# Performance work log

Hardware: AMD Instinct MI355X
Metric: run time of the kernel (lower is better)

The kernel has to match this reference:

```python
import jax, jax.numpy as jnp
import numpy as np

NUM_NODES = 200000
NUM_EDGES = 200000
NUM_GRAPHS = 2048
F_IN = 128
H = 64


def setup_inputs() -> dict:
    key = jax.random.key(0)
    ks = jax.random.split(key, 16)
    x = jax.random.normal(ks[0], (NUM_NODES, F_IN), dtype=jnp.float32)
    edge_index = jax.random.randint(ks[1], (2, NUM_EDGES), 0, NUM_NODES, dtype=jnp.int64)
    batch = jnp.sort(jax.random.randint(ks[2], (NUM_NODES,), 0, NUM_GRAPHS, dtype=jnp.int64))
    s_in = 1.0 / np.sqrt(F_IN)
    s_h = 1.0 / np.sqrt(H)
    W1a = jax.random.uniform(ks[3], (F_IN, H), jnp.float32, -s_in, s_in)
    b1a = jax.random.uniform(ks[4], (H,), jnp.float32, -s_in, s_in)
    W1b = jax.random.uniform(ks[5], (H, H), jnp.float32, -s_h, s_h)
    b1b = jax.random.uniform(ks[6], (H,), jnp.float32, -s_h, s_h)
    W2a = jax.random.uniform(ks[7], (H, H), jnp.float32, -s_h, s_h)
    b2a = jax.random.uniform(ks[8], (H,), jnp.float32, -s_h, s_h)
    W2b = jax.random.uniform(ks[9], (H, H), jnp.float32, -s_h, s_h)
    b2b = jax.random.uniform(ks[10], (H,), jnp.float32, -s_h, s_h)
    fcW = jax.random.uniform(ks[11], (H, 1), jnp.float32, -s_h, s_h)
    fcb = jax.random.uniform(ks[12], (1,), jnp.float32, -s_h, s_h)
    return {"x": x, "edge_index": edge_index, "batch": batch,
            "W1a": W1a, "b1a": b1a, "W1b": W1b, "b1b": b1b,
            "W2a": W2a, "b2a": b2a, "W2b": W2b, "b2b": b2b,
            "fcW": fcW, "fcb": fcb}


def gin_conv(h, edge_index, Wa, ba, Wb, bb):
    # sum aggregation: messages from source (row 0) scattered to target (row 1)
    msgs = h[edge_index[0]]  # [E, D]
    agg = jax.ops.segment_sum(msgs, edge_index[1], num_segments=NUM_NODES)
    z = h + agg  # eps = 0 default: (1+eps)*x + sum_j x_j
    z = jnp.maximum(z @ Wa + ba, 0.0)
    return z @ Wb + bb


def reference(x, edge_index, batch, W1a, b1a, W1b, b1b, W2a, b2a, W2b, b2b, fcW, fcb):
    h = jnp.maximum(gin_conv(x, edge_index, W1a, b1a, W1b, b1b), 0.0)
    h = jnp.maximum(gin_conv(h, edge_index, W2a, b2a, W2b, b2b), 0.0)
    # global mean pool per graph
    sums = jax.ops.segment_sum(h, batch, num_segments=NUM_GRAPHS)  # [G, H]
    counts = jax.ops.segment_sum(jnp.ones((h.shape[0],), h.dtype), batch, num_segments=NUM_GRAPHS)
    pooled = sums / jnp.maximum(counts, 1.0)[:, None]
    out = pooled @ fcW + fcb  # [G, 1]
    return out.squeeze(-1)
```

## Files before the change

kernel.cpp:

```cpp
#include <hip/hip_runtime.h>
#include <hip/hip_bf16.h>


#define NODES 200000
#define NPAD  200064
#define EDGES 200000
#define GRAPHS 2048
#define NB_SCAN 782

typedef __attribute__((ext_vector_type(8))) short short8;
typedef __attribute__((ext_vector_type(4))) short short4v;
typedef __attribute__((ext_vector_type(4))) float f32x4;

__device__ __forceinline__ unsigned short f2bf(float f) {
    unsigned u = __builtin_bit_cast(unsigned, f);
    u = (u + 0x7fffu + ((u >> 16) & 1u)) >> 16;
    return (unsigned short)u;
}
__device__ __forceinline__ float bf2f(unsigned short h) {
    unsigned u = ((unsigned)h) << 16;
    return __builtin_bit_cast(float, u);
}

__global__ __launch_bounds__(256) void count_k(
    const int* __restrict__ ei, int* __restrict__ cnt, int E)
{
    int e = blockIdx.x * 256 + threadIdx.x;
    if (e < E) atomicAdd(&cnt[ei[E + e]], 1);
}

__global__ __launch_bounds__(256) void scan1_k(
    const int* __restrict__ cnt, int* __restrict__ excl,
    int* __restrict__ bsum, int N)
{
    __shared__ int sh[256];
    int tid = threadIdx.x;
    int i = blockIdx.x * 256 + tid;
    int v = (i < N) ? cnt[i] : 0;
    sh[tid] = v;
    __syncthreads();
    for (int off = 1; off < 256; off <<= 1) {
        int t = (tid >= off) ? sh[tid - off] : 0;
        __syncthreads();
        sh[tid] += t;
        __syncthreads();
    }
    if (i < N) excl[i] = sh[tid] - v;
    if (tid == 255) bsum[blockIdx.x] = sh[255];
}

__global__ __launch_bounds__(1024) void scan2_k(int* __restrict__ bsum, int NB)
{
    __shared__ int sh[1024];
    int tid = threadIdx.x;
    int v = (tid < NB) ? bsum[tid] : 0;
    sh[tid] = v;
    __syncthreads();
    for (int off = 1; off < 1024; off <<= 1) {
        int t = (tid >= off) ? sh[tid - off] : 0;
        __syncthreads();
        sh[tid] += t;
        __syncthreads();
    }
    if (tid < NB) bsum[tid] = sh[tid] - v;
}

__global__ __launch_bounds__(256) void scan3_k(
    int* __restrict__ rowptr, const int* __restrict__ bsum,
    int* __restrict__ cursor, int N, int E)
{
    int i = blockIdx.x * 256 + threadIdx.x;
    if (i < N) {
        int v = rowptr[i] + bsum[blockIdx.x];
        rowptr[i] = v;
        cursor[i] = v;
    }
    if (i == 0) rowptr[N] = E;
}

__global__ __launch_bounds__(256) void fill_k(
    const int* __restrict__ ei, int* __restrict__ cursor,
    int* __restrict__ srcs, int E)
{
    int e = blockIdx.x * 256 + threadIdx.x;
    if (e < E) {
        int d = ei[E + e];
        int p = atomicAdd(&cursor[d], 1);
        srcs[p] = ei[e];
    }
}

__device__ __forceinline__ void wconv(const float* __restrict__ W,
                                      short* __restrict__ F, int e, int NE)
{
    int lane = e & 63, nb = (e >> 6) & 3, kc = e >> 8;
    int col = nb * 16 + (lane & 15);
    int kb = kc * 32 + ((lane >> 4) * 8);
    short8 hi, lo;
    #pragma unroll
    for (int j = 0; j < 8; ++j) {
        float w = W[(size_t)(kb + j) * 64 + col];
        unsigned short h = f2bf(w);
        float r = w - bf2f(h);
        hi[j] = (short)h;
        lo[j] = (short)f2bf(r);
    }
    *reinterpret_cast<short8*>(F + (size_t)e * 8) = hi;
    *reinterpret_cast<short8*>(F + (size_t)NE * 8 + (size_t)e * 8) = lo;
}

__global__ __launch_bounds__(256) void wsplit_k(
    const float* __restrict__ W1a, const float* __restrict__ W1b,
    const float* __restrict__ W2a, const float* __restrict__ W2b,
    short* __restrict__ F1a, short* __restrict__ F1b,
    short* __restrict__ F2a, short* __restrict__ F2b)
{
    int t = blockIdx.x * 256 + threadIdx.x;
    if (t < 1024)      wconv(W1a, F1a, t, 1024);
    else if (t < 1536) wconv(W1b, F1b, t - 1024, 512);
    else if (t < 2048) wconv(W2a, F2a, t - 1536, 512);
    else if (t < 2560) wconv(W2b, F2b, t - 2048, 512);
}

__device__ __forceinline__ void cvt_a8(const float4& a, const float4& b,
                                       short8& hi, short8& lo)
{
    float av[8] = {a.x, a.y, a.z, a.w, b.x, b.y, b.z, b.w};
    #pragma unroll
    for (int j = 0; j < 8; ++j) {
        unsigned short h = f2bf(av[j]);
        float r = av[j] - bf2f(h);
        hi[j] = (short)h;
        lo[j] = (short)f2bf(r);
    }
}

__global__ __launch_bounds__(256) void mm1_k(
    const float* __restrict__ A, const short* __restrict__ Wf,
    float* __restrict__ out, int N)
{
    const int tid = threadIdx.x;
    const int lane = tid & 63;
    const int wv = tid >> 6;
    const int row0w = blockIdx.x * 128 + wv * 32;
    const int grp = lane >> 4, c = lane & 15;
    const int koff = grp * 8;

    const float* Ar0 = A + (size_t)min(row0w + c, N - 1) * 128;
    const float* Ar1 = A + (size_t)min(row0w + 16 + c, N - 1) * 128;

    f32x4 acc[2][4];
    #pragma unroll
    for (int rg = 0; rg < 2; ++rg)
        #pragma unroll
        for (int nb = 0; nb < 4; ++nb)
            acc[rg][nb] = (f32x4){0.f, 0.f, 0.f, 0.f};

    #pragma unroll
    for (int kc = 0; kc < 4; ++kc) {
        const int kb = kc * 32 + koff;
        float4 a00 = *reinterpret_cast<const float4*>(Ar0 + kb);
        float4 a01 = *reinterpret_cast<const float4*>(Ar0 + kb + 4);
        float4 a10 = *reinterpret_cast<const float4*>(Ar1 + kb);
        float4 a11 = *reinterpret_cast<const float4*>(Ar1 + kb + 4);
        short8 h0, l0, h1, l1;
        cvt_a8(a00, a01, h0, l0);
        cvt_a8(a10, a11, h1, l1);
        #pragma unroll
        for (int nb = 0; nb < 4; ++nb) {
            short8 whi = *reinterpret_cast<const short8*>(Wf + ((size_t)((kc * 4 + nb) * 64) + lane) * 8);
            short8 wlo = *reinterpret_cast<const short8*>(Wf + ((size_t)(1024 + (kc * 4 + nb) * 64) + lane) * 8);
            acc[0][nb] = __builtin_amdgcn_mfma_f32_16x16x32_bf16(h0, whi, acc[0][nb], 0, 0, 0);
            acc[0][nb] = __builtin_amdgcn_mfma_f32_16x16x32_bf16(l0, whi, acc[0][nb], 0, 0, 0);
            acc[0][nb] = __builtin_amdgcn_mfma_f32_16x16x32_bf16(h0, wlo, acc[0][nb], 0, 0, 0);
            acc[1][nb] = __builtin_amdgcn_mfma_f32_16x16x32_bf16(h1, whi, acc[1][nb], 0, 0, 0);
            acc[1][nb] = __builtin_amdgcn_mfma_f32_16x16x32_bf16(l1, whi, acc[1][nb], 0, 0, 0);
            acc[1][nb] = __builtin_amdgcn_mfma_f32_16x16x32_bf16(h1, wlo, acc[1][nb], 0, 0, 0);
        }
    }

    #pragma unroll
    for (int rg = 0; rg < 2; ++rg)
        #pragma unroll
        for (int nb = 0; nb < 4; ++nb)
            #pragma unroll
            for (int reg = 0; reg < 4; ++reg)
                out[(size_t)(row0w + rg * 16 + grp * 4 + reg) * 64 + nb * 16 + c] = acc[rg][nb][reg];
}

__global__ __launch_bounds__(256) void agg_split_k(
    const float* __restrict__ y, const int* __restrict__ rowptr,
    const int* __restrict__ srcs, const float* __restrict__ bias,
    short* __restrict__ zHi, short* __restrict__ zLo, int N)
{
    int t = blockIdx.x * 256 + threadIdx.x;
    int node = t >> 4;
    if (node >= N) return;
    int c = (t & 15) * 4;

    int s0 = rowptr[node];
    int s1 = rowptr[node + 1];

    float4 acc = *reinterpret_cast<const float4*>(y + (size_t)node * 64 + c);
    float4 b4 = *reinterpret_cast<const float4*>(bias + c);
    acc.x += b4.x; acc.y += b4.y; acc.z += b4.z; acc.w += b4.w;

    for (int j = s0; j < s1; ++j) {
        int s = srcs[j];
        float4 vv = *reinterpret_cast<const float4*>(y + (size_t)s * 64 + c);
        acc.x += vv.x; acc.y += vv.y; acc.z += vv.z; acc.w += vv.w;
    }

    float v[4] = {fmaxf(acc.x, 0.f), fmaxf(acc.y, 0.f),
                  fmaxf(acc.z, 0.f), fmaxf(acc.w, 0.f)};
    short4v hv, lv;
    #pragma unroll
    for (int i = 0; i < 4; ++i) {
        unsigned short h = f2bf(v[i]);
        float r = v[i] - bf2f(h);
        hv[i] = (short)h;
        lv[i] = (short)f2bf(r);
    }
    *reinterpret_cast<short4v*>(zHi + (size_t)node * 64 + c) = hv;
    *reinterpret_cast<short4v*>(zLo + (size_t)node * 64 + c) = lv;
}

__device__ __forceinline__ void mm64_core(
    const short* __restrict__ zHi, const short* __restrict__ zLo,
    const short* __restrict__ Wf, int row0w, int lane, f32x4 acc[2][4])
{
    const int grp = lane >> 4, c = lane & 15;
    const int koff = grp * 8;
    const short* zh0 = zHi + (size_t)(row0w + c) * 64;
    const short* zl0 = zLo + (size_t)(row0w + c) * 64;
    const short* zh1 = zHi + (size_t)(row0w + 16 + c) * 64;
    const short* zl1 = zLo + (size_t)(row0w + 16 + c) * 64;

    #pragma unroll
    for (int kc = 0; kc < 2; ++kc) {
        const int kb = kc * 32 + koff;
        short8 h0 = *reinterpret_cast<const short8*>(zh0 + kb);
        short8 l0 = *reinterpret_cast<const short8*>(zl0 + kb);
        short8 h1 = *reinterpret_cast<const short8*>(zh1 + kb);
        short8 l1 = *reinterpret_cast<const short8*>(zl1 + kb);
        #pragma unroll
        for (int nb = 0; nb < 4; ++nb) {
            short8 whi = *reinterpret_cast<const short8*>(Wf + ((size_t)((kc * 4 + nb) * 64) + lane) * 8);
            short8 wlo = *reinterpret_cast<const short8*>(Wf + ((size_t)(512 + (kc * 4 + nb) * 64) + lane) * 8);
            acc[0][nb] = __builtin_amdgcn_mfma_f32_16x16x32_bf16(h0, whi, acc[0][nb], 0, 0, 0);
            acc[0][nb] = __builtin_amdgcn_mfma_f32_16x16x32_bf16(l0, whi, acc[0][nb], 0, 0, 0);
            acc[0][nb] = __builtin_amdgcn_mfma_f32_16x16x32_bf16(h0, wlo, acc[0][nb], 0, 0, 0);
            acc[1][nb] = __builtin_amdgcn_mfma_f32_16x16x32_bf16(h1, whi, acc[1][nb], 0, 0, 0);
            acc[1][nb] = __builtin_amdgcn_mfma_f32_16x16x32_bf16(l1, whi, acc[1][nb], 0, 0, 0);
            acc[1][nb] = __builtin_amdgcn_mfma_f32_16x16x32_bf16(h1, wlo, acc[1][nb], 0, 0, 0);
        }
    }
}

__global__ __launch_bounds__(256) void mmmm_k(
    const short* __restrict__ zHi, const short* __restrict__ zLo,
    const short* __restrict__ Wf1, const float* __restrict__ b1,
    const short* __restrict__ Wf2, float* __restrict__ out)
{
    __shared__ short hT[4][32 * 72];
    __shared__ short lT[4][32 * 72];
    const int tid = threadIdx.x;
    const int lane = tid & 63;
    const int wv = tid >> 6;
    const int row0w = blockIdx.x * 128 + wv * 32;
    const int grp = lane >> 4, c = lane & 15;
    const int koff = grp * 8;

    f32x4 acc[2][4];
    #pragma unroll
    for (int rg = 0; rg < 2; ++rg)
        #pragma unroll
        for (int nb = 0; nb < 4; ++nb)
            acc[rg][nb] = (f32x4){0.f, 0.f, 0.f, 0.f};

    mm64_core(zHi, zLo, Wf1, row0w, lane, acc);

    #pragma unroll
    for (int rg = 0; rg < 2; ++rg)
        #pragma unroll
        for (int nb = 0; nb < 4; ++nb) {
            const int col = nb * 16 + c;
            const float bv = b1[col];
            #pragma unroll
            for (int reg = 0; reg < 4; ++reg) {
                const int lr = rg * 16 + grp * 4 + reg;
                float v = fmaxf(acc[rg][nb][reg] + bv, 0.f);
                unsigned short h = f2bf(v);
                float r = v - bf2f(h);
                hT[wv][lr * 72 + col] = (short)h;
                lT[wv][lr * 72 + col] = (short)f2bf(r);
            }
        }
    __syncthreads();

    f32x4 acc2[2][4];
    #pragma unroll
    for (int rg = 0; rg < 2; ++rg)
        #pragma unroll
        for (int nb = 0; nb < 4; ++nb)
            acc2[rg][nb] = (f32x4){0.f, 0.f, 0.f, 0.f};

    #pragma unroll
    for (int kc = 0; kc < 2; ++kc) {
        const int kb = kc * 32 + koff;
        short8 h0 = *reinterpret_cast<const short8*>(&hT[wv][(0 + c) * 72 + kb]);
        short8 l0 = *reinterpret_cast<const short8*>(&lT[wv][(0 + c) * 72 + kb]);
        short8 h1 = *reinterpret_cast<const short8*>(&hT[wv][(16 + c) * 72 + kb]);
        short8 l1 = *reinterpret_cast<const short8*>(&lT[wv][(16 + c) * 72 + kb]);
        #pragma unroll
        for (int nb = 0; nb < 4; ++nb) {
            short8 whi = *reinterpret_cast<const short8*>(Wf2 + ((size_t)((kc * 4 + nb) * 64) + lane) * 8);
            short8 wlo = *reinterpret_cast<const short8*>(Wf2 + ((size_t)(512 + (kc * 4 + nb) * 64) + lane) * 8);
            acc2[0][nb] = __builtin_amdgcn_mfma_f32_16x16x32_bf16(h0, whi, acc2[0][nb], 0, 0, 0);
            acc2[0][nb] = __builtin_amdgcn_mfma_f32_16x16x32_bf16(l0, whi, acc2[0][nb], 0, 0, 0);
            acc2[0][nb] = __builtin_amdgcn_mfma_f32_16x16x32_bf16(h0, wlo, acc2[0][nb], 0, 0, 0);
            acc2[1][nb] = __builtin_amdgcn_mfma_f32_16x16x32_bf16(h1, whi, acc2[1][nb], 0, 0, 0);
            acc2[1][nb] = __builtin_amdgcn_mfma_f32_16x16x32_bf16(l1, whi, acc2[1][nb], 0, 0, 0);
            acc2[1][nb] = __builtin_amdgcn_mfma_f32_16x16x32_bf16(h1, wlo, acc2[1][nb], 0, 0, 0);
        }
    }

    #pragma unroll
    for (int rg = 0; rg < 2; ++rg)
        #pragma unroll
        for (int nb = 0; nb < 4; ++nb)
            #pragma unroll
            for (int reg = 0; reg < 4; ++reg)
                out[(size_t)(row0w + rg * 16 + grp * 4 + reg) * 64 + nb * 16 + c] = acc2[rg][nb][reg];
}

__global__ __launch_bounds__(256) void mmpool_k(
    const short* __restrict__ zHi, const short* __restrict__ zLo,
    const short* __restrict__ Wf, const float* __restrict__ bias,
    const float* __restrict__ fcW, const int* __restrict__ batch,
    float* __restrict__ gacc, int N)
{
    __shared__ float rd[4][32];
    __shared__ int bls[4][32];
    const int tid = threadIdx.x;
    const int lane = tid & 63;
    const int wv = tid >> 6;
    const int row0w = blockIdx.x * 128 + wv * 32;
    const int grp = lane >> 4, c = lane & 15;

    f32x4 acc[2][4];
    #pragma unroll
    for (int rg = 0; rg < 2; ++rg)
        #pragma unroll
        for (int nb = 0; nb < 4; ++nb)
            acc[rg][nb] = (f32x4){0.f, 0.f, 0.f, 0.f};

    mm64_core(zHi, zLo, Wf, row0w, lane, acc);

    float bv[4], fw[4];
    #pragma unroll
    for (int nb = 0; nb < 4; ++nb) {
        bv[nb] = bias[nb * 16 + c];
        fw[nb] = fcW[nb * 16 + c];
    }
    if (lane < 32) bls[wv][lane] = batch[min(row0w + lane, N - 1)];

    #pragma unroll
    for (int rg = 0; rg < 2; ++rg)
        #pragma unroll
        for (int reg = 0; reg < 4; ++reg) {
            float t = 0.f;
            #pragma unroll
            for (int nb = 0; nb < 4; ++nb)
                t += fmaxf(acc[rg][nb][reg] + bv[nb], 0.f) * fw[nb];
            t += __shfl_xor(t, 1, 16);
            t += __shfl_xor(t, 2, 16);
            t += __shfl_xor(t, 4, 16);
            t += __shfl_xor(t, 8, 16);
            if (c == 0) rd[wv][rg * 16 + grp * 4 + reg] = t;
        }

    if (lane == 0) {
        int cnt = min(32, N - row0w);
        if (cnt > 0) {
            int curg = bls[wv][0];
            float s = rd[wv][0];
            for (int i = 1; i < cnt; ++i) {
                int g = bls[wv][i];
                float v = rd[wv][i];
                if (g == curg) s += v;
                else { atomicAdd(&gacc[curg], s); curg = g; s = v; }
            }
            atomicAdd(&gacc[curg], s);
        }
    }
}

__global__ __launch_bounds__(256) void finalize_k(
    const float* __restrict__ gacc, const int* __restrict__ batch,
    const float* __restrict__ fcb, float* __restrict__ out, int N, int G)
{
    int g = blockIdx.x * 256 + threadIdx.x;
    if (g >= G) return;
    int lo = 0, hi = N;
    while (lo < hi) { int m = (lo + hi) >> 1; if (batch[m] < g) lo = m + 1; else hi = m; }
    int start = lo;
    hi = N;
    while (lo < hi) { int m = (lo + hi) >> 1; if (batch[m] < g + 1) lo = m + 1; else hi = m; }
    float cnt = fmaxf((float)(lo - start), 1.f);
    out[g] = gacc[g] / cnt + fcb[0];
}

extern "C" void kernel_launch(void* const* d_in, const int* in_sizes, int n_in,
                              void* d_out, int out_size, void* d_ws, size_t ws_size,
                              hipStream_t stream)
{
    const float* x     = (const float*)d_in[0];
    const int*   ei    = (const int*)d_in[1];
    const int*   batch = (const int*)d_in[2];
    const float* W1a   = (const float*)d_in[3];
    const float* b1a   = (const float*)d_in[4];
    const float* W1b   = (const float*)d_in[5];
    const float* b1b   = (const float*)d_in[6];
    const float* W2a   = (const float*)d_in[7];
    const float* b2a   = (const float*)d_in[8];
    const float* W2b   = (const float*)d_in[9];
    const float* b2b   = (const float*)d_in[10];
    const float* fcW   = (const float*)d_in[11];
    const float* fcb   = (const float*)d_in[12];
    float* out = (float*)d_out;

    const int N = NODES, E = EDGES, G = GRAPHS;
    char* ws = (char*)d_ws;

    float* yBuf = (float*)ws;
    short* zHi  = (short*)(ws + (size_t)NPAD * 64 * 4);
    short* zLo  = zHi + (size_t)NPAD * 64;
    char*  rest = (char*)(zLo + (size_t)NPAD * 64);
    int* cnt    = (int*)rest;
    int* rowptr = cnt + NODES;
    int* cursor = rowptr + NODES + 1;
    int* srcs   = cursor + NODES;
    int* bsum   = srcs + EDGES;
    float* gacc = (float*)(bsum + NB_SCAN + 2);
    short* F1a  = (short*)(((size_t)(gacc + GRAPHS) + 63) & ~(size_t)63);
    short* F1b  = F1a + 2 * 1024 * 8;
    short* F2a  = F1b + 2 * 512 * 8;
    short* F2b  = F2a + 2 * 512 * 8;

    const int NBLK = NPAD / 128;

    hipMemsetAsync(cnt, 0, (size_t)N * sizeof(int), stream);
    hipMemsetAsync(gacc, 0, (size_t)G * sizeof(float), stream);
    count_k<<<NB_SCAN, 256, 0, stream>>>(ei, cnt, E);
    scan1_k<<<NB_SCAN, 256, 0, stream>>>(cnt, rowptr, bsum, N);
    scan2_k<<<1, 1024, 0, stream>>>(bsum, NB_SCAN);
    scan3_k<<<NB_SCAN, 256, 0, stream>>>(rowptr, bsum, cursor, N, E);
    fill_k<<<NB_SCAN, 256, 0, stream>>>(ei, cursor, srcs, E);
    wsplit_k<<<10, 256, 0, stream>>>(W1a, W1b, W2a, W2b, F1a, F1b, F2a, F2b);

    mm1_k<<<NBLK, 256, 0, stream>>>(x, F1a, yBuf, N);
    agg_split_k<<<N * 16 / 256, 256, 0, stream>>>(yBuf, rowptr, srcs, b1a, zHi, zLo, N);

    mmmm_k<<<NBLK, 256, 0, stream>>>(zHi, zLo, F1b, b1b, F2a, yBuf);

    agg_split_k<<<N * 16 / 256, 256, 0, stream>>>(yBuf, rowptr, srcs, b2a, zHi, zLo, N);

    mmpool_k<<<NBLK, 256, 0, stream>>>(zHi, zLo, F2b, b2b, fcW, batch, gacc, N);
    finalize_k<<<(G + 255) / 256, 256, 0, stream>>>(gacc, batch, fcb, out, N, G);
}
```

Baseline: 328.8 us.

## Fuse neighbor aggregation into the following MFMA matmul kernels

The separate aggregation kernels that wrote bf16 hi/lo split buffers to global memory are removed. Each lane of the matmul kernels now gathers its own 16-element MFMA fragment straight from the fp32 y buffer plus neighbor rows via CSR, applies bias and ReLU, splits to hi/lo in registers, and feeds the MFMAs directly. This drops two kernel launches and the zHi/zLo write-and-reread traffic. In exchange, the gather runs with lower parallelism per node (one lane per node fragment with uncoalesced row reads), and a separate y2 buffer is needed.

```diff
diff --git a/kernel.cpp b/kernel.cpp
--- a/kernel.cpp
+++ b/kernel.cpp
@@ -9,7 +9,6 @@
 #define NB_SCAN 782
 
 typedef __attribute__((ext_vector_type(8))) short short8;
-typedef __attribute__((ext_vector_type(4))) short short4v;
 typedef __attribute__((ext_vector_type(4))) float f32x4;
 
 __device__ __forceinline__ unsigned short f2bf(float f) {
@@ -188,79 +187,61 @@
                 out[(size_t)(row0w + rg * 16 + grp * 4 + reg) * 64 + nb * 16 + c] = acc[rg][nb][reg];
 }
 
-__global__ __launch_bounds__(256) void agg_split_k(
+__device__ __forceinline__ void agg_frag16(
     const float* __restrict__ y, const int* __restrict__ rowptr,
     const int* __restrict__ srcs, const float* __restrict__ bias,
-    short* __restrict__ zHi, short* __restrict__ zLo, int N)
-{
-    int t = blockIdx.x * 256 + threadIdx.x;
-    int node = t >> 4;
-    if (node >= N) return;
-    int c = (t & 15) * 4;
-
-    int s0 = rowptr[node];
-    int s1 = rowptr[node + 1];
-
-    float4 acc = *reinterpret_cast<const float4*>(y + (size_t)node * 64 + c);
-    float4 b4 = *reinterpret_cast<const float4*>(bias + c);
-    acc.x += b4.x; acc.y += b4.y; acc.z += b4.z; acc.w += b4.w;
-
+    int n, int koff, bool valid, short8 fh[2], short8 fl[2])
+{
+    if (!valid) {
+        #pragma unroll
+        for (int i = 0; i < 8; ++i) {
+            fh[0][i] = 0; fl[0][i] = 0; fh[1][i] = 0; fl[1][i] = 0;
+        }
+        return;
+    }
+    float a[16];
+    {
+        const float* yr = y + (size_t)n * 64;
+        float4 a0 = *reinterpret_cast<const float4*>(yr + koff);
+        float4 a1 = *reinterpret_cast<const float4*>(yr + koff + 4);
+        float4 a2 = *reinterpret_cast<const float4*>(yr + 32 + koff);
+        float4 a3 = *reinterpret_cast<const float4*>(yr + 32 + koff + 4);
+        float4 b0 = *reinterpret_cast<const float4*>(bias + koff);
+        float4 b1 = *reinterpret_cast<const float4*>(bias + koff + 4);
+        float4 b2 = *reinterpret_cast<const float4*>(bias + 32 + koff);
+        float4 b3 = *reinterpret_cast<const float4*>(bias + 32 + koff + 4);
+        a[0] = a0.x + b0.x;  a[1] = a0.y + b0.y;  a[2] = a0.z + b0.z;  a[3] = a0.w + b0.w;
+        a[4] = a1.x + b1.x;  a[5] = a1.y + b1.y;  a[6] = a1.z + b1.z;  a[7] = a1.w + b1.w;
+        a[8] = a2.x + b2.x;  a[9] = a2.y + b2.y;  a[10] = a2.z + b2.z; a[11] = a2.w + b2.w;
+        a[12] = a3.x + b3.x; a[13] = a3.y + b3.y; a[14] = a3.z + b3.z; a[15] = a3.w + b3.w;
+    }
+    int s0 = rowptr[n], s1 = rowptr[n + 1];
     for (int j = s0; j < s1; ++j) {
-        int s = srcs[j];
-        float4 vv = *reinterpret_cast<const float4*>(y + (size_t)s * 64 + c);
-        acc.x += vv.x; acc.y += vv.y; acc.z += vv.z; acc.w += vv.w;
-    }
-
-    float v[4] = {fmaxf(acc.x, 0.f), fmaxf(acc.y, 0.f),
-                  fmaxf(acc.z, 0.f), fmaxf(acc.w, 0.f)};
-    short4v hv, lv;
-    #pragma unroll
-    for (int i = 0; i < 4; ++i) {
-        unsigned short h = f2bf(v[i]);
-        float r = v[i] - bf2f(h);
-        hv[i] = (short)h;
-        lv[i] = (short)f2bf(r);
-    }
-    *reinterpret_cast<short4v*>(zHi + (size_t)node * 64 + c) = hv;
-    *reinterpret_cast<short4v*>(zLo + (size_t)node * 64 + c) = lv;
-}
-
-__device__ __forceinline__ void mm64_core(
-    const short* __restrict__ zHi, const short* __restrict__ zLo,
-    const short* __restrict__ Wf, int row0w, int lane, f32x4 acc[2][4])
-{
-    const int grp = lane >> 4, c = lane & 15;
-    const int koff = grp * 8;
-    const short* zh0 = zHi + (size_t)(row0w + c) * 64;
-    const short* zl0 = zLo + (size_t)(row0w + c) * 64;
-    const short* zh1 = zHi + (size_t)(row0w + 16 + c) * 64;
-    const short* zl1 = zLo + (size_t)(row0w + 16 + c) * 64;
-
-    #pragma unroll
-    for (int kc = 0; kc < 2; ++kc) {
-        const int kb = kc * 32 + koff;
-        short8 h0 = *reinterpret_cast<const short8*>(zh0 + kb);
-        short8 l0 = *reinterpret_cast<const short8*>(zl0 + kb);
-        short8 h1 = *reinterpret_cast<const short8*>(zh1 + kb);
-        short8 l1 = *reinterpret_cast<const short8*>(zl1 + kb);
-        #pragma unroll
-        for (int nb = 0; nb < 4; ++nb) {
-            short8 whi = *reinterpret_cast<const short8*>(Wf + ((size_t)((kc * 4 + nb) * 64) + lane) * 8);
-            short8 wlo = *reinterpret_cast<const short8*>(Wf + ((size_t)(512 + (kc * 4 + nb) * 64) + lane) * 8);
-            acc[0][nb] = __builtin_amdgcn_mfma_f32_16x16x32_bf16(h0, whi, acc[0][nb], 0, 0, 0);
-            acc[0][nb] = __builtin_amdgcn_mfma_f32_16x16x32_bf16(l0, whi, acc[0][nb], 0, 0, 0);
-            acc[0][nb] = __builtin_amdgcn_mfma_f32_16x16x32_bf16(h0, wlo, acc[0][nb], 0, 0, 0);
-            acc[1][nb] = __builtin_amdgcn_mfma_f32_16x16x32_bf16(h1, whi, acc[1][nb], 0, 0, 0);
-            acc[1][nb] = __builtin_amdgcn_mfma_f32_16x16x32_bf16(l1, whi, acc[1][nb], 0, 0, 0);
-            acc[1][nb] = __builtin_amdgcn_mfma_f32_16x16x32_bf16(h1, wlo, acc[1][nb], 0, 0, 0);
-        }
-    }
-}
-
-__global__ __launch_bounds__(256) void mmmm_k(
-    const short* __restrict__ zHi, const short* __restrict__ zLo,
+        const float* ys = y + (size_t)srcs[j] * 64;
+        float4 v0 = *reinterpret_cast<const float4*>(ys + koff);
+        float4 v1 = *reinterpret_cast<const float4*>(ys + koff + 4);
+        float4 v2 = *reinterpret_cast<const float4*>(ys + 32 + koff);
+        float4 v3 = *reinterpret_cast<const float4*>(ys + 32 + koff + 4);
+        a[0] += v0.x;  a[1] += v0.y;  a[2] += v0.z;  a[3] += v0.w;
+        a[4] += v1.x;  a[5] += v1.y;  a[6] += v1.z;  a[7] += v1.w;
+        a[8] += v2.x;  a[9] += v2.y;  a[10] += v2.z; a[11] += v2.w;
+        a[12] += v3.x; a[13] += v3.y; a[14] += v3.z; a[15] += v3.w;
+    }
+    #pragma unroll
+    for (int i = 0; i < 16; ++i) {
+        float v = fmaxf(a[i], 0.f);
+        unsigned short h = f2bf(v);
+        float r = v - bf2f(h);
+        fh[i >> 3][i & 7] = (short)h;
+        fl[i >> 3][i & 7] = (short)f2bf(r);
+    }
+}
+
+__global__ __launch_bounds__(256) void mmaggmm_k(
+    const float* __restrict__ y, const int* __restrict__ rowptr,
+    const int* __restrict__ srcs, const float* __restrict__ bagg,
     const short* __restrict__ Wf1, const float* __restrict__ b1,
-    const short* __restrict__ Wf2, float* __restrict__ out)
+    const short* __restrict__ Wf2, float* __restrict__ out, int N)
 {
     __shared__ short hT[4][32 * 72];
     __shared__ short lT[4][32 * 72];
@@ -271,6 +252,14 @@
     const int grp = lane >> 4, c = lane & 15;
     const int koff = grp * 8;
 
+    short8 fh0[2], fl0[2], fh1[2], fl1[2];
+    {
+        int n0 = row0w + c;
+        int n1 = row0w + 16 + c;
+        agg_frag16(y, rowptr, srcs, bagg, n0, koff, n0 < N, fh0, fl0);
+        agg_frag16(y, rowptr, srcs, bagg, n1, koff, n1 < N, fh1, fl1);
+    }
+
     f32x4 acc[2][4];
     #pragma unroll
     for (int rg = 0; rg < 2; ++rg)
@@ -278,7 +267,20 @@
         for (int nb = 0; nb < 4; ++nb)
             acc[rg][nb] = (f32x4){0.f, 0.f, 0.f, 0.f};
 
-    mm64_core(zHi, zLo, Wf1, row0w, lane, acc);
+    #pragma unroll
+    for (int kc = 0; kc < 2; ++kc) {
+        #pragma unroll
+        for (int nb = 0; nb < 4; ++nb) {
+            short8 whi = *reinterpret_cast<const short8*>(Wf1 + ((size_t)((kc * 4 + nb) * 64) + lane) * 8);
+            short8 wlo = *reinterpret_cast<const short8*>(Wf1 + ((size_t)(512 + (kc * 4 + nb) * 64) + lane) * 8);
+            acc[0][nb] = __builtin_amdgcn_mfma_f32_16x16x32_bf16(fh0[kc], whi, acc[0][nb], 0, 0, 0);
+            acc[0][nb] = __builtin_amdgcn_mfma_f32_16x16x32_bf16(fl0[kc], whi, acc[0][nb], 0, 0, 0);
+            acc[0][nb] = __builtin_amdgcn_mfma_f32_16x16x32_bf16(fh0[kc], wlo, acc[0][nb], 0, 0, 0);
+            acc[1][nb] = __builtin_amdgcn_mfma_f32_16x16x32_bf16(fh1[kc], whi, acc[1][nb], 0, 0, 0);
+            acc[1][nb] = __builtin_amdgcn_mfma_f32_16x16x32_bf16(fl1[kc], whi, acc[1][nb], 0, 0, 0);
+            acc[1][nb] = __builtin_amdgcn_mfma_f32_16x16x32_bf16(fh1[kc], wlo, acc[1][nb], 0, 0, 0);
+        }
+    }
 
     #pragma unroll
     for (int rg = 0; rg < 2; ++rg)
@@ -334,8 +336,9 @@
                 out[(size_t)(row0w + rg * 16 + grp * 4 + reg) * 64 + nb * 16 + c] = acc2[rg][nb][reg];
 }
 
-__global__ __launch_bounds__(256) void mmpool_k(
-    const short* __restrict__ zHi, const short* __restrict__ zLo,
+__global__ __launch_bounds__(256) void mmaggpool_k(
+    const float* __restrict__ y, const int* __restrict__ rowptr,
+    const int* __restrict__ srcs, const float* __restrict__ bagg,
     const short* __restrict__ Wf, const float* __restrict__ bias,
     const float* __restrict__ fcW, const int* __restrict__ batch,
     float* __restrict__ gacc, int N)
@@ -347,6 +350,15 @@
     const int wv = tid >> 6;
     const int row0w = blockIdx.x * 128 + wv * 32;
     const int grp = lane >> 4, c = lane & 15;
+    const int koff = grp * 8;
+
+    short8 fh0[2], fl0[2], fh1[2], fl1[2];
+    {
+        int n0 = row0w + c;
+        int n1 = row0w + 16 + c;
+        agg_frag16(y, rowptr, srcs, bagg, n0, koff, n0 < N, fh0, fl0);
+        agg_frag16(y, rowptr, srcs, bagg, n1, koff, n1 < N, fh1, fl1);
+    }
 
     f32x4 acc[2][4];
     #pragma unroll
@@ -355,7 +367,20 @@
         for (int nb = 0; nb < 4; ++nb)
             acc[rg][nb] = (f32x4){0.f, 0.f, 0.f, 0.f};
 
-    mm64_core(zHi, zLo, Wf, row0w, lane, acc);
+    #pragma unroll
+    for (int kc = 0; kc < 2; ++kc) {
+        #pragma unroll
+        for (int nb = 0; nb < 4; ++nb) {
+            short8 whi = *reinterpret_cast<const short8*>(Wf + ((size_t)((kc * 4 + nb) * 64) + lane) * 8);
+            short8 wlo = *reinterpret_cast<const short8*>(Wf + ((size_t)(512 + (kc * 4 + nb) * 64) + lane) * 8);
+            acc[0][nb] = __builtin_amdgcn_mfma_f32_16x16x32_bf16(fh0[kc], whi, acc[0][nb], 0, 0, 0);
+            acc[0][nb] = __builtin_amdgcn_mfma_f32_16x16x32_bf16(fl0[kc], whi, acc[0][nb], 0, 0, 0);
+            acc[0][nb] = __builtin_amdgcn_mfma_f32_16x16x32_bf16(fh0[kc], wlo, acc[0][nb], 0, 0, 0);
+            acc[1][nb] = __builtin_amdgcn_mfma_f32_16x16x32_bf16(fh1[kc], whi, acc[1][nb], 0, 0, 0);
+            acc[1][nb] = __builtin_amdgcn_mfma_f32_16x16x32_bf16(fl1[kc], whi, acc[1][nb], 0, 0, 0);
+            acc[1][nb] = __builtin_amdgcn_mfma_f32_16x16x32_bf16(fh1[kc], wlo, acc[1][nb], 0, 0, 0);
+        }
+    }
 
     float bv[4], fw[4];
     #pragma unroll
@@ -433,10 +458,9 @@
     const int N = NODES, E = EDGES, G = GRAPHS;
     char* ws = (char*)d_ws;
 
-    float* yBuf = (float*)ws;
-    short* zHi  = (short*)(ws + (size_t)NPAD * 64 * 4);
-    short* zLo  = zHi + (size_t)NPAD * 64;
-    char*  rest = (char*)(zLo + (size_t)NPAD * 64);
+    float* y1 = (float*)ws;
+    float* y2 = (float*)(ws + (size_t)NPAD * 64 * 4);
+    char*  rest = ws + 2 * (size_t)NPAD * 64 * 4;
     int* cnt    = (int*)rest;
     int* rowptr = cnt + NODES;
     int* cursor = rowptr + NODES + 1;
@@ -459,13 +483,10 @@
     fill_k<<<NB_SCAN, 256, 0, stream>>>(ei, cursor, srcs, E);
     wsplit_k<<<10, 256, 0, stream>>>(W1a, W1b, W2a, W2b, F1a, F1b, F2a, F2b);
 
-    mm1_k<<<NBLK, 256, 0, stream>>>(x, F1a, yBuf, N);
-    agg_split_k<<<N * 16 / 256, 256, 0, stream>>>(yBuf, rowptr, srcs, b1a, zHi, zLo, N);
-
-    mmmm_k<<<NBLK, 256, 0, stream>>>(zHi, zLo, F1b, b1b, F2a, yBuf);
-
-    agg_split_k<<<N * 16 / 256, 256, 0, stream>>>(yBuf, rowptr, srcs, b2a, zHi, zLo, N);
-
-    mmpool_k<<<NBLK, 256, 0, stream>>>(zHi, zLo, F2b, b2b, fcW, batch, gacc, N);
+    mm1_k<<<NBLK, 256, 0, stream>>>(x, F1a, y1, N);
+
+    mmaggmm_k<<<NBLK, 256, 0, stream>>>(y1, rowptr, srcs, b1a, F1b, b1b, F2a, y2, N);
+
+    mmaggpool_k<<<NBLK, 256, 0, stream>>>(y2, rowptr, srcs, b2a, F2b, b2b, fcW, batch, gacc, N);
     finalize_k<<<(G + 255) / 256, 256, 0, stream>>>(gacc, batch, fcb, out, N, G);
 }
```

Measured after the change: 306.4 us. -6.8%, faster.
